# Kernel tuning notes

Hardware: AMD Instinct MI355X
Metric: run time of the kernel (lower is better)

Reference implementation:

```python
import jax, jax.numpy as jnp
import numpy as np

B, T, C, H = 2, 2048, 512, 8
HD = C // H  # head size = 64

def _layernorm(x, g, b, eps=1e-5):
    mu = jnp.mean(x, axis=-1, keepdims=True)
    var = jnp.var(x, axis=-1, keepdims=True)
    return (x - mu) * jax.lax.rsqrt(var + eps) * g + b

def setup_inputs() -> dict:
    key = jax.random.key(0)
    ks = jax.random.split(key, 12)
    s_attn = 1.0 / np.sqrt(C)
    s_proj = 1.0 / np.sqrt(H * HD)
    s_ffn1 = 1.0 / np.sqrt(C)
    s_ffn2 = 1.0 / np.sqrt(4 * C)
    return {
        "x":   jax.random.normal(ks[0], (B, T, C), jnp.float32),
        "Wq":  jax.random.uniform(ks[1], (H, C, HD), jnp.float32, -s_attn, s_attn),
        "Wk":  jax.random.uniform(ks[2], (H, C, HD), jnp.float32, -s_attn, s_attn),
        "Wv":  jax.random.uniform(ks[3], (H, C, HD), jnp.float32, -s_attn, s_attn),
        "Wo":  jax.random.uniform(ks[4], (H * HD, C), jnp.float32, -s_proj, s_proj),
        "bo":  jax.random.uniform(ks[5], (C,), jnp.float32, -s_proj, s_proj),
        "W1":  jax.random.uniform(ks[6], (C, 4 * C), jnp.float32, -s_ffn1, s_ffn1),
        "b1":  jax.random.uniform(ks[7], (4 * C,), jnp.float32, -s_ffn1, s_ffn1),
        "W2":  jax.random.uniform(ks[8], (4 * C, C), jnp.float32, -s_ffn2, s_ffn2),
        "b2":  jax.random.uniform(ks[9], (C,), jnp.float32, -s_ffn2, s_ffn2),
        "g1":  jnp.ones((C,), jnp.float32),
        "be1": jnp.zeros((C,), jnp.float32),
        "g2":  jnp.ones((C,), jnp.float32),
        "be2": jnp.zeros((C,), jnp.float32),
    }

def reference(x, Wq, Wk, Wv, Wo, bo, W1, b1, W2, b2, g1, be1, g2, be2):
    # --- multi-head causal self-attention on ln1(x) ---
    h = _layernorm(x, g1, be1)
    q = jnp.einsum("btc,hcd->bhtd", h, Wq)
    k = jnp.einsum("btc,hcd->bhtd", h, Wk)
    v = jnp.einsum("btc,hcd->bhtd", h, Wv)
    scores = jnp.einsum("bhtd,bhsd->bhts", q, k) * (HD ** -0.5)
    causal = jnp.tril(jnp.ones((T, T), bool))
    scores = jnp.where(causal, scores, -jnp.inf)
    wei = jax.nn.softmax(scores, axis=-1)
    attn = jnp.einsum("bhts,bhsd->bhtd", wei, v)
    attn = attn.transpose(0, 2, 1, 3).reshape(B, T, H * HD)  # concat heads
    x = x + attn @ Wo + bo
    # --- GELU MLP on ln2(x) ---
    h2 = _layernorm(x, g2, be2)
    ff = jax.nn.gelu(h2 @ W1 + b1, approximate=False) @ W2 + b2
    return x + ff
```

## Files before the change

### kernel.cpp

```cpp
#include <hip/hip_runtime.h>
#include <math.h>

constexpr int B_   = 2;
constexpr int T_   = 2048;
constexpr int C_   = 512;
constexpr int H_   = 8;
constexpr int HD_  = 64;
constexpr int M_   = B_ * T_;
constexpr int FF_  = 4 * C_;
constexpr int NQKV_ = 3 * C_;

typedef __attribute__((ext_vector_type(8))) short short8;
typedef __attribute__((ext_vector_type(4))) short short4v;
typedef __attribute__((ext_vector_type(4))) float floatx4;

static __device__ __forceinline__ unsigned short f2bf(float f) {
    union { float f; unsigned u; } v; v.f = f;
    unsigned r = v.u + 0x7fff + ((v.u >> 16) & 1);
    return (unsigned short)(r >> 16);
}

static __device__ __forceinline__ float bf2f(unsigned short s) {
    union { unsigned u; float f; } v; v.u = (unsigned)s << 16; return v.f;
}

static __device__ __forceinline__ unsigned packbf2(float a, float b) {
    union { float f; unsigned u; } x, y; x.f = a; y.f = b;
    unsigned lo = (x.u + 0x7fff + ((x.u >> 16) & 1)) >> 16;
    unsigned hi = (y.u + 0x7fff + ((y.u >> 16) & 1)) & 0xffff0000u;
    return lo | hi;
}

static __device__ __forceinline__ void gl2lds16(const unsigned short* g,
                                                unsigned short* l) {
    __builtin_amdgcn_global_load_lds(
        (const __attribute__((address_space(1))) void*)g,
        (__attribute__((address_space(3))) void*)l, 16, 0, 0);
}

#if __has_builtin(__builtin_amdgcn_mfma_f32_16x16x16bf16_1k)
static __device__ __forceinline__ floatx4 mfma16(short4v a, short4v b, floatx4 c) {
    return __builtin_amdgcn_mfma_f32_16x16x16bf16_1k(a, b, c, 0, 0, 0);
}
#elif __has_builtin(__builtin_amdgcn_mfma_f32_16x16x16_bf16)
static __device__ __forceinline__ floatx4 mfma16(short4v a, short4v b, floatx4 c) {
    return __builtin_amdgcn_mfma_f32_16x16x16_bf16(a, b, c, 0, 0, 0);
}
#else
static __device__ __forceinline__ floatx4 mfma16(short4v a, short4v b, floatx4 c) {
    asm volatile("v_mfma_f32_16x16x16_bf16 %0, %1, %2, %0"
                 : "+v"(c) : "v"(a), "v"(b));
    return c;
}
#endif

static __device__ __forceinline__ void ln_row(int row, int lane,
                                              const float* __restrict__ x,
                                              const float* __restrict__ g,
                                              const float* __restrict__ b,
                                              unsigned short* __restrict__ out,
                                              const float* __restrict__ badd,
                                              float* __restrict__ xmut) {
    const float* xr = x + (size_t)row * C_;
    int c0 = lane * 8;
    float4 v0 = *(const float4*)(xr + c0);
    float4 v1 = *(const float4*)(xr + c0 + 4);
    float vals[8] = {v0.x, v0.y, v0.z, v0.w, v1.x, v1.y, v1.z, v1.w};

    float s = 0.f, ss = 0.f;
#pragma unroll
    for (int j = 0; j < 8; j++) { s += vals[j]; ss += vals[j] * vals[j]; }
#pragma unroll
    for (int off = 32; off; off >>= 1) {
        s  += __shfl_xor(s,  off);
        ss += __shfl_xor(ss, off);
    }
    float mu  = s / C_;
    float var = ss / C_ - mu * mu;
    float rs  = rsqrtf(var + 1e-5f);

    unsigned short* orow = out + (size_t)row * C_;
#pragma unroll
    for (int j = 0; j < 8; j++) {
        int c = c0 + j;
        orow[c] = f2bf((vals[j] - mu) * rs * g[c] + b[c]);
    }
    if (badd) {
        float* xw = xmut + (size_t)row * C_;
        float4 w0, w1;
        w0.x = vals[0] + badd[c0];     w0.y = vals[1] + badd[c0 + 1];
        w0.z = vals[2] + badd[c0 + 2]; w0.w = vals[3] + badd[c0 + 3];
        w1.x = vals[4] + badd[c0 + 4]; w1.y = vals[5] + badd[c0 + 5];
        w1.z = vals[6] + badd[c0 + 6]; w1.w = vals[7] + badd[c0 + 7];
        *(float4*)(xw + c0)     = w0;
        *(float4*)(xw + c0 + 4) = w1;
    }
}

__global__ __launch_bounds__(256) void prologue(
        const float* __restrict__ Wq, const float* __restrict__ Wk,
        const float* __restrict__ Wv, const float* __restrict__ Wo,
        const float* __restrict__ W1, const float* __restrict__ W2,
        const float* __restrict__ x,  const float* __restrict__ g1,
        const float* __restrict__ be1,
        unsigned short* __restrict__ Wqkv_t, unsigned short* __restrict__ Wo_t,
        unsigned short* __restrict__ W1_t,   unsigned short* __restrict__ W2_t,
        unsigned short* __restrict__ hb) {
    int idx = blockIdx.x;
    int tid = threadIdx.x;
    if (idx >= 3072) {
        int row = (idx - 3072) * 4 + (tid >> 6);
        ln_row(row, tid & 63, x, g1, be1, hb, nullptr, nullptr);
        return;
    }
    __shared__ float tile[32][33];
    const float* src; unsigned short* dst;
    int K, N, k0, n0;
    float scale = 1.0f;
    if (idx < 768) {
        int wz = idx >> 8, rem = idx & 255;
        int h = rem >> 5, r2 = rem & 31;
        k0 = (r2 >> 1) * 32; n0 = (r2 & 1) * 32;
        src = (wz == 0 ? Wq : (wz == 1 ? Wk : Wv)) + (size_t)h * C_ * HD_;
        dst = Wqkv_t + (size_t)(wz * C_ + h * HD_) * C_;
        K = C_; N = HD_;
        if (wz == 0) scale = 0.125f;
    } else if (idx < 1024) {
        int rem = idx - 768;
        n0 = (rem & 15) * 32; k0 = (rem >> 4) * 32;
        src = Wo; dst = Wo_t; K = C_; N = C_;
    } else if (idx < 2048) {
        int rem = idx - 1024;
        n0 = (rem & 63) * 32; k0 = (rem >> 6) * 32;
        src = W1; dst = W1_t; K = C_; N = FF_;
    } else {
        int rem = idx - 2048;
        n0 = (rem & 15) * 32; k0 = (rem >> 4) * 32;
        src = W2; dst = W2_t; K = FF_; N = C_;
    }
    int tx = tid & 31, ty = tid >> 5;
#pragma unroll
    for (int i = 0; i < 4; i++)
        tile[ty + i * 8][tx] = src[(size_t)(k0 + ty + i * 8) * N + n0 + tx];
    __syncthreads();
#pragma unroll
    for (int i = 0; i < 4; i++)
        dst[(size_t)(n0 + ty + i * 8) * K + k0 + tx] = f2bf(tile[tx][ty + i * 8] * scale);
}

__global__ __launch_bounds__(256) void ln_kernel(
        const float* __restrict__ x, const float* __restrict__ g,
        const float* __restrict__ b, unsigned short* __restrict__ out,
        const float* __restrict__ badd, float* __restrict__ xmut) {
    int tid = threadIdx.x;
    int row = blockIdx.x * 4 + (tid >> 6);
    ln_row(row, tid & 63, x, g, b, out, badd, xmut);
}

template<int BM, int BN, int BK>
__global__ __launch_bounds__(256) void mfma_gemm(
        const unsigned short* __restrict__ A,
        const unsigned short* __restrict__ Bt,
        const float* __restrict__ bias,
        const float* __restrict__ resid,
        float* __restrict__ outF,
        unsigned short* __restrict__ outB,
        unsigned short* __restrict__ vT,
        const float* __restrict__ lP,
        int M, int N, int K, int flags) {
    constexpr int WM = BM / 2, WN = BN / 2;
    constexpr int MI = WM / 16, NI = WN / 16, KH = BK / 32;
    __shared__ unsigned short smem[KH * (BM + BN) * 32];
    unsigned short* As = smem;
    unsigned short* Bs = smem + KH * BM * 32;

    int t = threadIdx.x;
    int lane = t & 63, w = t >> 6;
    int wr = (w >> 1) * WM, wc = (w & 1) * WN;
    int lm = lane & 15, lq = lane >> 4;
    int m0 = blockIdx.y * BM, n0 = blockIdx.x * BN;
    int kper = K / gridDim.z;
    int kbeg = blockIdx.z * kper, kend = kbeg + kper;

    floatx4 acc[MI][NI];
#pragma unroll
    for (int mi = 0; mi < MI; mi++)
#pragma unroll
        for (int ni = 0; ni < NI; ni++) acc[mi][ni] = (floatx4){0.f, 0.f, 0.f, 0.f};

    for (int k0 = kbeg; k0 < kend; k0 += BK) {
        __syncthreads();
        if (flags & 32) {
#pragma unroll
            for (int hh = 0; hh < KH; hh++) {
#pragma unroll
                for (int j = 0; j < BM * 4 / 256; j++) {
                    int i = t + j * 256;
                    int gr = m0 + (i >> 2);
                    int f = k0 + hh * 32 + (i & 3) * 8;
                    const unsigned short* pa = A + (size_t)gr * K + f;
                    short8 a8 = *(const short8*)pa;
                    short8 b8 = *(const short8*)(pa + (size_t)M_ * C_);
                    float l0 = lP[(size_t)gr * H_ + (f >> 6)];
                    float l1 = lP[(size_t)(M_ + gr) * H_ + (f >> 6)];
                    float inv = 1.f / (l0 + l1);
                    unsigned pk[4];
#pragma unroll
                    for (int q = 0; q < 4; q++) {
                        float v0 = (bf2f((unsigned short)a8[2 * q]) +
                                    bf2f((unsigned short)b8[2 * q])) * inv;
                        float v1 = (bf2f((unsigned short)a8[2 * q + 1]) +
                                    bf2f((unsigned short)b8[2 * q + 1])) * inv;
                        pk[q] = packbf2(v0, v1);
                    }
                    *(short8*)&As[hh * BM * 32 + i * 8] = *(short8*)pk;
                }
            }
        } else {
#pragma unroll
            for (int hh = 0; hh < KH; hh++)
#pragma unroll
                for (int j = 0; j < BM * 4 / 256; j++) {
                    int i = t + j * 256;
                    gl2lds16(A + (size_t)(m0 + (i >> 2)) * K + k0 + hh * 32 + (i & 3) * 8,
                             &As[hh * BM * 32 + i * 8]);
                }
        }
#pragma unroll
        for (int hh = 0; hh < KH; hh++)
#pragma unroll
            for (int j = 0; j < BN * 4 / 256; j++) {
                int i = t + j * 256;
                gl2lds16(Bt + (size_t)(n0 + (i >> 2)) * K + k0 + hh * 32 + (i & 3) * 8,
                         &Bs[hh * BN * 32 + i * 8]);
            }
        __syncthreads();

#pragma unroll
        for (int hh = 0; hh < KH; hh++) {
            short8 af[MI], bfv[NI];
#pragma unroll
            for (int mi = 0; mi < MI; mi++)
                af[mi] = *(const short8*)&As[hh * BM * 32 + (wr + mi * 16 + lm) * 32 + lq * 8];
#pragma unroll
            for (int ni = 0; ni < NI; ni++)
                bfv[ni] = *(const short8*)&Bs[hh * BN * 32 + (wc + ni * 16 + lm) * 32 + lq * 8];
#pragma unroll
            for (int mi = 0; mi < MI; mi++)
#pragma unroll
                for (int ni = 0; ni < NI; ni++)
                    acc[mi][ni] = __builtin_amdgcn_mfma_f32_16x16x32_bf16(
                        af[mi], bfv[ni], acc[mi][ni], 0, 0, 0);
        }
    }

    if ((flags & 16) && n0 >= 2 * C_) {
        __syncthreads();
        unsigned short* Ts = smem;
#pragma unroll
        for (int mi = 0; mi < MI; mi++)
#pragma unroll
            for (int ni = 0; ni < NI; ni++) {
                int cl = wc + ni * 16 + lm;
#pragma unroll
                for (int r = 0; r < 4; r++)
                    Ts[cl * 72 + wr + mi * 16 + lq * 4 + r] = f2bf(acc[mi][ni][r]);
            }
        __syncthreads();
        int b = m0 >> 11, trow = m0 & (T_ - 1);
#pragma unroll
        for (int it = 0; it < BN * (BM / 8) / 256; it++) {
            int u = it * 256 + t;
            int cl = u >> 3, seg = u & 7;
            int vcol = n0 - 2 * C_ + cl;
            int hh2 = vcol >> 6, dd = vcol & 63;
            short8 vv = *(const short8*)&Ts[cl * 72 + seg * 8];
            *(short8*)&vT[(size_t)((b * H_ + hh2) * HD_ + dd) * T_ + trow + seg * 8] = vv;
        }
        return;
    }

    if (flags & 64) {
#pragma unroll
        for (int mi = 0; mi < MI; mi++)
#pragma unroll
            for (int ni = 0; ni < NI; ni++) {
                int gc = n0 + wc + ni * 16 + lm;
#pragma unroll
                for (int r = 0; r < 4; r++) {
                    int gr = m0 + wr + mi * 16 + lq * 4 + r;
                    atomicAdd(&outF[(size_t)gr * N + gc], acc[mi][ni][r]);
                }
            }
        return;
    }

#pragma unroll
    for (int mi = 0; mi < MI; mi++)
#pragma unroll
        for (int ni = 0; ni < NI; ni++) {
            int gc = n0 + wc + ni * 16 + lm;
#pragma unroll
            for (int r = 0; r < 4; r++) {
                int gr = m0 + wr + mi * 16 + lq * 4 + r;
                float v = acc[mi][ni][r];
                if (flags & 1) v += bias[gc];
                if (flags & 4) v = 0.5f * v * (1.0f + erff(v * 0.70710678118654752f));
                if (flags & 2) v += resid[(size_t)gr * N + gc];
                if (flags & 8) outB[(size_t)gr * N + gc] = f2bf(v);
                else           outF[(size_t)gr * N + gc] = v;
            }
        }
}

__global__ __launch_bounds__(256, 4) void attn_mfma(
        const unsigned short* __restrict__ qkv,
        const unsigned short* __restrict__ vT,
        unsigned short* __restrict__ oP,
        float* __restrict__ lP) {
    __shared__ unsigned short Ks[2][64 * 72];
    __shared__ unsigned short Vt[2][64 * 72];

    int t = threadIdx.x;
    int wq = t >> 6, lane = t & 63;
    int lm = lane & 15, quad = lane >> 4;
    int bh = blockIdx.y, b = bh >> 3, h = bh & 7;
    int tile = blockIdx.x >> 1, s = blockIdx.x & 1;
    int q0 = tile * 64;

    int srow = t >> 2, sq4 = t & 3;

    const unsigned short* kbase = qkv + (size_t)(b * T_) * NQKV_ + C_ + h * HD_;
    const unsigned short* vbase = vT + (size_t)(bh * HD_ + srow) * T_;

    int gq_row = q0 + wq * 16 + lm;
    const unsigned short* qp = qkv + (size_t)(b * T_ + gq_row) * NQKV_ + h * HD_;
    short8 qf0 = *(const short8*)(qp + quad * 8);
    short8 qf1 = *(const short8*)(qp + 32 + quad * 8);

    float l_s = 0.f;
    floatx4 o_acc[4];
#pragma unroll
    for (int dt = 0; dt < 4; dt++) o_acc[dt] = (floatx4){0.f, 0.f, 0.f, 0.f};

    short8 kp0, kp1, vp0, vp1;
    if (s <= tile) {
        int s0 = s * 64;
        const unsigned short* kg = kbase + (size_t)(s0 + srow) * NQKV_ + sq4 * 16;
        kp0 = *(const short8*)kg;
        kp1 = *(const short8*)(kg + 8);
        vp0 = *(const short8*)(vbase + s0 + sq4 * 16);
        vp1 = *(const short8*)(vbase + s0 + sq4 * 16 + 8);
        *(short8*)&Ks[0][srow * 72 + sq4 * 16]     = kp0;
        *(short8*)&Ks[0][srow * 72 + sq4 * 16 + 8] = kp1;
        *(short8*)&Vt[0][srow * 72 + sq4 * 16]     = vp0;
        *(short8*)&Vt[0][srow * 72 + sq4 * 16 + 8] = vp1;
    }

    int buf = 0;
    for (int c = s; c <= tile; c += 2) {
        bool havenext = (c + 2 <= tile);
        if (havenext) {
            int s0n = (c + 2) * 64;
            const unsigned short* kgn = kbase + (size_t)(s0n + srow) * NQKV_ + sq4 * 16;
            kp0 = *(const short8*)kgn;
            kp1 = *(const short8*)(kgn + 8);
            vp0 = *(const short8*)(vbase + s0n + sq4 * 16);
            vp1 = *(const short8*)(vbase + s0n + sq4 * 16 + 8);
        }
        __syncthreads();

        bool diag = (c == tile);
#pragma unroll
        for (int kt = 0; kt < 4; kt++) {
            if (diag && kt > wq) continue;
            short8 kf0 = *(const short8*)&Ks[buf][(kt * 16 + lm) * 72 + quad * 8];
            short8 kf1 = *(const short8*)&Ks[buf][(kt * 16 + lm) * 72 + 32 + quad * 8];
            floatx4 sv = (floatx4){0.f, 0.f, 0.f, 0.f};
            sv = __builtin_amdgcn_mfma_f32_16x16x32_bf16(kf0, qf0, sv, 0, 0, 0);
            sv = __builtin_amdgcn_mfma_f32_16x16x32_bf16(kf1, qf1, sv, 0, 0, 0);
            float p0, p1, p2, p3;
            {
                bool e = diag && (kt == wq);
                p0 = (e && (quad * 4 + 0 > lm)) ? 0.f : __expf(sv[0]);
                p1 = (e && (quad * 4 + 1 > lm)) ? 0.f : __expf(sv[1]);
                p2 = (e && (quad * 4 + 2 > lm)) ? 0.f : __expf(sv[2]);
                p3 = (e && (quad * 4 + 3 > lm)) ? 0.f : __expf(sv[3]);
            }
            l_s += (p0 + p1) + (p2 + p3);
            uint2 pu;
            pu.x = packbf2(p0, p1);
            pu.y = packbf2(p2, p3);
            short4v pk = *(short4v*)&pu;
#pragma unroll
            for (int dt = 0; dt < 4; dt++) {
                short4v vf = *(const short4v*)&Vt[buf][(dt * 16 + lm) * 72 + kt * 16 + quad * 4];
                o_acc[dt] = mfma16(pk, vf, o_acc[dt]);
            }
        }
        if (havenext) {
            int nb = buf ^ 1;
            *(short8*)&Ks[nb][srow * 72 + sq4 * 16]     = kp0;
            *(short8*)&Ks[nb][srow * 72 + sq4 * 16 + 8] = kp1;
            *(short8*)&Vt[nb][srow * 72 + sq4 * 16]     = vp0;
            *(short8*)&Vt[nb][srow * 72 + sq4 * 16 + 8] = vp1;
        }
        buf ^= 1;
    }

    float lsum = l_s;
    lsum += __shfl_xor(lsum, 16);
    lsum += __shfl_xor(lsum, 32);
    if (quad == 0)
        lP[(size_t)s * M_ * H_ + (size_t)(b * T_ + q0 + wq * 16 + lm) * H_ + h] = lsum;
    unsigned short* obase = oP + (size_t)s * M_ * C_;
#pragma unroll
    for (int r = 0; r < 4; r++) {
        int gq = q0 + wq * 16 + quad * 4 + r;
        unsigned short* op = obase + (size_t)(b * T_ + gq) * C_ + h * HD_ + lm;
#pragma unroll
        for (int dt = 0; dt < 4; dt++)
            op[dt * 16] = f2bf(o_acc[dt][r]);
    }
}

extern "C" void kernel_launch(void* const* d_in, const int* in_sizes, int n_in,
                              void* d_out, int out_size, void* d_ws, size_t ws_size,
                              hipStream_t stream) {
    const float* x   = (const float*)d_in[0];
    const float* Wq  = (const float*)d_in[1];
    const float* Wk  = (const float*)d_in[2];
    const float* Wv  = (const float*)d_in[3];
    const float* Wo  = (const float*)d_in[4];
    const float* bo  = (const float*)d_in[5];
    const float* W1  = (const float*)d_in[6];
    const float* b1  = (const float*)d_in[7];
    const float* W2  = (const float*)d_in[8];
    const float* b2  = (const float*)d_in[9];
    const float* g1  = (const float*)d_in[10];
    const float* be1 = (const float*)d_in[11];
    const float* g2  = (const float*)d_in[12];
    const float* be2 = (const float*)d_in[13];
    float* out = (float*)d_out;

    unsigned short* Wqkv_t = (unsigned short*)d_ws;
    unsigned short* Wo_t   = Wqkv_t + (size_t)NQKV_ * C_;
    unsigned short* W1_t   = Wo_t   + (size_t)C_ * C_;
    unsigned short* W2_t   = W1_t   + (size_t)C_ * FF_;
    unsigned short* hb     = W2_t   + (size_t)FF_ * C_;
    unsigned short* attnb  = hb     + (size_t)M_ * C_;
    unsigned short* qkvb   = attnb  + (size_t)M_ * C_;
    unsigned short* vTb    = qkvb   + (size_t)M_ * NQKV_;
    unsigned short* oPb    = vTb    + (size_t)M_ * C_;
    float*          lPf    = (float*)(oPb + 2 * (size_t)M_ * C_);
    unsigned short* ff1    = attnb;

    prologue<<<4096, 256, 0, stream>>>(Wq, Wk, Wv, Wo, W1, W2, x, g1, be1,
                                       Wqkv_t, Wo_t, W1_t, W2_t, hb);

    mfma_gemm<64, 128, 64><<<dim3(NQKV_ / 128, M_ / 64), 256, 0, stream>>>(
        hb, Wqkv_t, nullptr, nullptr, nullptr, qkvb, vTb, nullptr,
        M_, NQKV_, C_, 8 | 16);

    attn_mfma<<<dim3(64, B_ * H_), 256, 0, stream>>>(qkvb, vTb, oPb, lPf);

    mfma_gemm<64, 64, 64><<<dim3(C_ / 64, M_ / 64), 256, 0, stream>>>(
        oPb, Wo_t, bo, x, out, nullptr, nullptr, lPf, M_, C_, C_, 1 | 2 | 32);

    ln_kernel<<<M_ / 4, 256, 0, stream>>>(out, g2, be2, hb, b2, out);

    mfma_gemm<128, 128, 64><<<dim3(FF_ / 128, M_ / 128), 256, 0, stream>>>(
        hb, W1_t, b1, nullptr, nullptr, ff1, nullptr, nullptr,
        M_, FF_, C_, 1 | 4 | 8);

    mfma_gemm<128, 128, 64><<<dim3(C_ / 128, M_ / 128, 4), 256, 0, stream>>>(
        ff1, W2_t, nullptr, nullptr, out, nullptr, nullptr, nullptr,
        M_, C_, FF_, 64);
}
```

Baseline: 233.8 us.

## Replace split-K atomic FFN2 with direct bias+residual epilogue, retile FFN GEMMs

Removes the split-K (z=4) atomicAdd path for the second FFN GEMM, which required the layernorm kernel to pre-write x+b2 into the output. The FFN2 GEMM now uses 64x64 tiles over the full K with a plain bias-plus-residual epilogue, and the FFN1 GEMM moves from 128x128 to 64x128 tiles. This drops the atomic traffic and the extra residual store, but gives FFN2 fewer K-parallel blocks (512 blocks each looping over K=2048) and smaller tiles with less data reuse.

```diff
diff --git a/kernel.cpp b/kernel.cpp
--- a/kernel.cpp
+++ b/kernel.cpp
@@ -58,9 +58,7 @@
                                               const float* __restrict__ x,
                                               const float* __restrict__ g,
                                               const float* __restrict__ b,
-                                              unsigned short* __restrict__ out,
-                                              const float* __restrict__ badd,
-                                              float* __restrict__ xmut) {
+                                              unsigned short* __restrict__ out) {
     const float* xr = x + (size_t)row * C_;
     int c0 = lane * 8;
     float4 v0 = *(const float4*)(xr + c0);
@@ -84,16 +82,6 @@
     for (int j = 0; j < 8; j++) {
         int c = c0 + j;
         orow[c] = f2bf((vals[j] - mu) * rs * g[c] + b[c]);
-    }
-    if (badd) {
-        float* xw = xmut + (size_t)row * C_;
-        float4 w0, w1;
-        w0.x = vals[0] + badd[c0];     w0.y = vals[1] + badd[c0 + 1];
-        w0.z = vals[2] + badd[c0 + 2]; w0.w = vals[3] + badd[c0 + 3];
-        w1.x = vals[4] + badd[c0 + 4]; w1.y = vals[5] + badd[c0 + 5];
-        w1.z = vals[6] + badd[c0 + 6]; w1.w = vals[7] + badd[c0 + 7];
-        *(float4*)(xw + c0)     = w0;
-        *(float4*)(xw + c0 + 4) = w1;
     }
 }
 
@@ -110,7 +98,7 @@
     int tid = threadIdx.x;
     if (idx >= 3072) {
         int row = (idx - 3072) * 4 + (tid >> 6);
-        ln_row(row, tid & 63, x, g1, be1, hb, nullptr, nullptr);
+        ln_row(row, tid & 63, x, g1, be1, hb);
         return;
     }
     __shared__ float tile[32][33];
@@ -150,11 +138,10 @@
 
 __global__ __launch_bounds__(256) void ln_kernel(
         const float* __restrict__ x, const float* __restrict__ g,
-        const float* __restrict__ b, unsigned short* __restrict__ out,
-        const float* __restrict__ badd, float* __restrict__ xmut) {
+        const float* __restrict__ b, unsigned short* __restrict__ out) {
     int tid = threadIdx.x;
     int row = blockIdx.x * 4 + (tid >> 6);
-    ln_row(row, tid & 63, x, g, b, out, badd, xmut);
+    ln_row(row, tid & 63, x, g, b, out);
 }
 
 template<int BM, int BN, int BK>
@@ -179,8 +166,6 @@
     int wr = (w >> 1) * WM, wc = (w & 1) * WN;
     int lm = lane & 15, lq = lane >> 4;
     int m0 = blockIdx.y * BM, n0 = blockIdx.x * BN;
-    int kper = K / gridDim.z;
-    int kbeg = blockIdx.z * kper, kend = kbeg + kper;
 
     floatx4 acc[MI][NI];
 #pragma unroll
@@ -188,7 +173,7 @@
 #pragma unroll
         for (int ni = 0; ni < NI; ni++) acc[mi][ni] = (floatx4){0.f, 0.f, 0.f, 0.f};
 
-    for (int k0 = kbeg; k0 < kend; k0 += BK) {
+    for (int k0 = 0; k0 < K; k0 += BK) {
         __syncthreads();
         if (flags & 32) {
 #pragma unroll
@@ -277,21 +262,6 @@
             short8 vv = *(const short8*)&Ts[cl * 72 + seg * 8];
             *(short8*)&vT[(size_t)((b * H_ + hh2) * HD_ + dd) * T_ + trow + seg * 8] = vv;
         }
-        return;
-    }
-
-    if (flags & 64) {
-#pragma unroll
-        for (int mi = 0; mi < MI; mi++)
-#pragma unroll
-            for (int ni = 0; ni < NI; ni++) {
-                int gc = n0 + wc + ni * 16 + lm;
-#pragma unroll
-                for (int r = 0; r < 4; r++) {
-                    int gr = m0 + wr + mi * 16 + lq * 4 + r;
-                    atomicAdd(&outF[(size_t)gr * N + gc], acc[mi][ni][r]);
-                }
-            }
         return;
     }
 
@@ -467,13 +437,13 @@
     mfma_gemm<64, 64, 64><<<dim3(C_ / 64, M_ / 64), 256, 0, stream>>>(
         oPb, Wo_t, bo, x, out, nullptr, nullptr, lPf, M_, C_, C_, 1 | 2 | 32);
 
-    ln_kernel<<<M_ / 4, 256, 0, stream>>>(out, g2, be2, hb, b2, out);
-
-    mfma_gemm<128, 128, 64><<<dim3(FF_ / 128, M_ / 128), 256, 0, stream>>>(
+    ln_kernel<<<M_ / 4, 256, 0, stream>>>(out, g2, be2, hb);
+
+    mfma_gemm<64, 128, 64><<<dim3(FF_ / 128, M_ / 64), 256, 0, stream>>>(
         hb, W1_t, b1, nullptr, nullptr, ff1, nullptr, nullptr,
         M_, FF_, C_, 1 | 4 | 8);
 
-    mfma_gemm<128, 128, 64><<<dim3(C_ / 128, M_ / 128, 4), 256, 0, stream>>>(
-        ff1, W2_t, nullptr, nullptr, out, nullptr, nullptr, nullptr,
-        M_, C_, FF_, 64);
-}
+    mfma_gemm<64, 64, 64><<<dim3(C_ / 64, M_ / 64), 256, 0, stream>>>(
+        ff1, W2_t, b2, out, out, nullptr, nullptr, nullptr,
+        M_, C_, FF_, 1 | 2);
+}
```

Measured after the change: 219.7 us. 1.06x faster.
